# Optimization experiments

Measured on AMD Instinct MI355X. Metric: run time of the kernel, lower is better.

## Reference

```python
import jax, jax.numpy as jnp
import numpy as np
from jax import lax

IN_CH = 32
OUT_CH = 32
K = 7
PAD = 3
STRIDE = 1


def setup_inputs() -> dict:
    key = jax.random.key(0)
    k1, k2, k3 = jax.random.split(key, 3)
    B, T = 4, 4096
    x = jax.random.normal(k1, (B, IN_CH, T), dtype=jnp.float32)
    # weight-generating conv params: [out*in*k, in, k]
    fan_in = IN_CH * K
    W = jax.random.normal(k2, (OUT_CH * IN_CH * K, IN_CH, K), dtype=jnp.float32) / np.sqrt(fan_in).astype(np.float32)
    b = jax.random.normal(k3, (OUT_CH * IN_CH * K,), dtype=jnp.float32) * 0.01
    return {"x": x, "W": W, "b": b}


def _unfold1d(x):
    # x: [B, C, L]; pad then stack K shifted views -> [B, C, K, T]
    xp = jnp.pad(x, ((0, 0), (0, 0), (PAD, PAD)))
    Lp = xp.shape[-1]
    T = Lp - K + 1
    return jnp.stack([xp[:, :, i:i + T:STRIDE] for i in range(K)], axis=2)


def reference(x, W, b):
    B, C, L = x.shape
    # dynamic weight generation: conv1d, same padding -> [B, out*in*K, T]
    dw = lax.conv_general_dilated(
        x, W, window_strides=(STRIDE,), padding=[(PAD, PAD)],
        dimension_numbers=("NCH", "OIH", "NCH"))
    dw = dw + b[None, :, None]
    dw = dw.reshape(B, OUT_CH, IN_CH, K, -1)  # [B, O, I, K, T]
    dw = jax.nn.softmax(dw / np.sqrt(K).astype(np.float32), axis=3)
    x_unf = _unfold1d(x)  # [B, I, K, T]
    y = jnp.einsum("bckt,bockt->bot", x_unf, dw)
    return y
```

## Files before the change

kernel.cpp:

```cpp
#include <hip/hip_runtime.h>
#include <hip/hip_bf16.h>


typedef unsigned short u16;
typedef unsigned int u32;
typedef __attribute__((ext_vector_type(8))) short short8;
typedef __attribute__((ext_vector_type(4))) float f32x4;

#define IN_CH 32
#define OUT_CH 32
#define KW 7
#define TSZ 4096
#define BSZ 4
#define CONTR 224
#define NROWS 7168
#define BLK_T 512
#define XS_STRIDE 40
#define XS_ROWS (BLK_T + 6)
#define SLICE_U16 3584
#define CH_U16 25088
#define CEXP2 0.54528747f

__device__ __forceinline__ u32 f2bf(float v) {
    u32 b = __float_as_uint(v);
    return (b + 0x7fffu + ((b >> 16) & 1u)) >> 16;
}

__device__ __forceinline__ void glds16(const u16* g, u16* l) {
    __builtin_amdgcn_global_load_lds((__attribute__((address_space(1))) void*)g,
                                     (__attribute__((address_space(3))) void*)l,
                                     16, 0, 0);
}

__global__ __launch_bounds__(512)
void wprep(const float* __restrict__ W, const float* __restrict__ bias,
           u16* __restrict__ Wp, float* __restrict__ bp) {
    __shared__ float ws[CH_U16];
    int ch  = blockIdx.x;
    int tid = threadIdx.x;
    const float* src = W + (size_t)ch * CH_U16;
    #pragma unroll
    for (int it = 0; it < 49; ++it)
        ws[it * 512 + tid] = src[it * 512 + tid];
    __syncthreads();
    u16* dst = Wp + (size_t)ch * CH_U16;
    #pragma unroll
    for (int it = 0; it < 49; ++it) {
        int oidx = it * 512 + tid;
        int e  = oidx & 7;
        int pp = (oidx >> 3) & 3;
        int t1 = oidx >> 5;
        int rp = t1 % 112;
        int j  = t1 / 112;
        int p  = pp ^ ((rp >> 1) & 3);
        int c  = p * 8 + e;
        int k  = rp >> 4;
        int q  = rp & 15;
        dst[oidx] = (u16)f2bf(ws[(q * 7 + k) * CONTR + c * 7 + j] * CEXP2);
    }
    if (tid < 112) {
        int k = tid >> 4, q = tid & 15;
        int gp = ch * 16 + q;
        int o = gp >> 5, i = gp & 31;
        bp[ch * 112 + tid] = bias[(o * IN_CH + i) * KW + k] * CEXP2;
    }
}

__global__ __launch_bounds__(256)
void xprep(const float* __restrict__ x, u16* __restrict__ xT) {
    int bid = blockIdx.x;
    int b = bid >> 6;
    int t0 = (bid & 63) * 64;
    __shared__ float lds[32][65];
    int tid = threadIdx.x;
    #pragma unroll
    for (int it = 0; it < 8; ++it) {
        int gi = it * 256 + tid;
        int c = gi >> 6;
        int t = gi & 63;
        lds[c][t] = x[((size_t)b * IN_CH + c) * TSZ + t0 + t];
    }
    __syncthreads();
    #pragma unroll
    for (int it = 0; it < 4; ++it) {
        int wi = it * 256 + tid;
        int t  = wi >> 4;
        int cp = wi & 15;
        u32 b0 = f2bf(lds[cp * 2][t]);
        u32 b1 = f2bf(lds[cp * 2 + 1][t]);
        ((u32*)xT)[((size_t)b * TSZ + t0 + t) * 16 + cp] = b0 | (b1 << 16);
    }
}

__global__ __launch_bounds__(512, 1)
void dconv_main(const u16* __restrict__ Wp, const float* __restrict__ bp,
                const u16* __restrict__ xT, float* __restrict__ out) {
    __shared__ u16 xs[XS_ROWS * XS_STRIDE];
    __shared__ u16 wbuf[2][CH_U16];

    int tid  = threadIdx.x;
    int lane = tid & 63;
    int wave = tid >> 6;
    int g    = lane >> 4;
    int col  = lane & 15;

    int bid = blockIdx.x;
    int b   = bid & 3;
    int tt  = (bid >> 2) & 7;
    int os  = bid >> 5;
    int t0  = tt * BLK_T;

    #pragma unroll
    for (int it = 0; it < 17; ++it) {
        int wi = it * 512 + tid;
        if (wi < XS_ROWS * 16) {
            int row = wi >> 4;
            int cp  = wi & 15;
            int t = t0 - 3 + row;
            u32 v = 0;
            if (t >= 0 && t < TSZ)
                v = ((const u32*)xT)[((size_t)b * TSZ + t) * 16 + cp];
            int sw = ((row >> 3) & 1) << 3;
            *(u32*)&xs[row * XS_STRIDE + ((cp * 2) ^ sw)] = v;
        }
    }

    if (wave < 7) {
        const u16* src = Wp + (size_t)(os * 8) * CH_U16 + wave * SLICE_U16 + lane * 8;
        u16* dst = &wbuf[0][wave * SLICE_U16];
        #pragma unroll
        for (int it = 0; it < 7; ++it) glds16(src + it * 512, dst + it * 512);
    }
    __syncthreads();

    int laneA = col * 32 + ((g ^ ((col >> 1) & 3)) * 8);
    int colw0 = wave * 64 + col;

    float yacc[4] = {0.f, 0.f, 0.f, 0.f};

    #pragma unroll 1
    for (int ci = 0; ci < 8; ++ci) {
        int cur = ci & 1;
        if (ci < 7 && wave < 7) {
            const u16* src = Wp + (size_t)(os * 8 + ci + 1) * CH_U16 + wave * SLICE_U16 + lane * 8;
            u16* dst = &wbuf[cur ^ 1][wave * SLICE_U16];
            #pragma unroll
            for (int it = 0; it < 7; ++it) glds16(src + it * 512, dst + it * 512);
        }

        int ch = os * 8 + ci;
        int cc = ci & 1;

        f32x4 acc[7][4];
        const float* bsrc = bp + ch * 112 + g * 4;
        #pragma unroll
        for (int m = 0; m < 7; ++m) {
            f32x4 bv = *(const f32x4*)(bsrc + m * 16);
            acc[m][0] = bv; acc[m][1] = bv; acc[m][2] = bv; acc[m][3] = bv;
        }

        __builtin_amdgcn_s_setprio(1);
        const u16* wl = &wbuf[cur][laneA];
        #pragma unroll
        for (int j = 0; j < 7; ++j) {
            short8 bf[4];
            #pragma unroll
            for (int ct = 0; ct < 4; ++ct) {
                int row = colw0 + ct * 16 + j;
                int sw = ((row >> 3) & 1) << 3;
                bf[ct] = *(const short8*)&xs[row * XS_STRIDE + ((g * 8) ^ sw)];
            }
            #pragma unroll
            for (int m = 0; m < 7; ++m) {
                short8 af = *(const short8*)(wl + j * SLICE_U16 + m * 512);
                acc[m][0] = __builtin_amdgcn_mfma_f32_16x16x32_bf16(af, bf[0], acc[m][0], 0, 0, 0);
                acc[m][1] = __builtin_amdgcn_mfma_f32_16x16x32_bf16(af, bf[1], acc[m][1], 0, 0, 0);
                acc[m][2] = __builtin_amdgcn_mfma_f32_16x16x32_bf16(af, bf[2], acc[m][2], 0, 0, 0);
                acc[m][3] = __builtin_amdgcn_mfma_f32_16x16x32_bf16(af, bf[3], acc[m][3], 0, 0, 0);
            }
        }
        __builtin_amdgcn_s_setprio(0);

        __syncthreads();

        int ibase = cc * 16 + g * 4;
        #pragma unroll
        for (int ct = 0; ct < 4; ++ct) {
            int colw = colw0 + ct * 16;
            u32 xv0[7], xv1[7];
            #pragma unroll
            for (int k = 0; k < 7; ++k) {
                int row = colw + k;
                int sw = ((row >> 3) & 1) << 3;
                const u32* px = (const u32*)&xs[row * XS_STRIDE + (ibase ^ sw)];
                xv0[k] = px[0]; xv1[k] = px[1];
            }
            #pragma unroll
            for (int r = 0; r < 4; ++r) {
                float ssum = 0.f, psum = 0.f;
                #pragma unroll
                for (int k = 0; k < 7; ++k) {
                    float e = __builtin_amdgcn_exp2f(acc[k][ct][r]);
                    u32 w = (r & 2) ? xv1[k] : xv0[k];
                    float xf = __uint_as_float((r & 1) ? (w & 0xffff0000u) : (w << 16));
                    ssum += e;
                    psum = fmaf(e, xf, psum);
                }
                yacc[ct] += psum * __builtin_amdgcn_rcpf(ssum);
            }
        }

        if (cc == 1) {
            int o = os * 4 + (ci >> 1);
            #pragma unroll
            for (int ct = 0; ct < 4; ++ct) {
                float v = yacc[ct];
                v += __shfl_xor(v, 16, 64);
                v += __shfl_xor(v, 32, 64);
                if (lane < 16)
                    out[((size_t)b * OUT_CH + o) * TSZ + t0 + wave * 64 + ct * 16 + col] = v;
                yacc[ct] = 0.f;
            }
        }
    }
}

extern "C" void kernel_launch(void* const* d_in, const int* in_sizes, int n_in,
                              void* d_out, int out_size, void* d_ws, size_t ws_size,
                              hipStream_t stream) {
    const float* x    = (const float*)d_in[0];
    const float* W    = (const float*)d_in[1];
    const float* bias = (const float*)d_in[2];
    float* out = (float*)d_out;

    u16*   Wp = (u16*)d_ws;
    float* bp = (float*)((char*)d_ws + 3211264);
    u16*   xT = (u16*)((char*)d_ws + 3211264 + 28672);

    hipLaunchKernelGGL(wprep, dim3(64), dim3(512), 0, stream, W, bias, Wp, bp);
    hipLaunchKernelGGL(xprep, dim3(BSZ * (TSZ / 64)), dim3(256), 0, stream, x, xT);
    hipLaunchKernelGGL(dconv_main, dim3(256), dim3(512), 0, stream, Wp, bp, xT, out);
}
```

Before: 122.3 us.

## Interleave weight prefetch with per-tap MFMA phases and permute channel order

Spreads the next-channel weight global→LDS staging across the seven tap iterations instead of issuing it all at the start. Each tap now loads its A/B fragments, waits at a workgroup barrier, then runs its MFMA burst. The channel order is permuted consistently in wprep and xprep so the epilogue can reuse the same LDS addressing as the MFMA B-fragment loads. This aims to overlap weight transfers with compute and keep waves in lockstep, but adds two barriers per tap, which may cost more than it saves.

Result: slower. 132.9 us (+8.6%).

```diff
diff --git a/kernel.cpp b/kernel.cpp
--- a/kernel.cpp
+++ b/kernel.cpp
@@ -53,7 +53,7 @@
         int rp = t1 % 112;
         int j  = t1 / 112;
         int p  = pp ^ ((rp >> 1) & 3);
-        int c  = p * 8 + e;
+        int c  = ((e >> 2) << 4) + (p << 2) + (e & 3);
         int k  = rp >> 4;
         int q  = rp & 15;
         dst[oidx] = (u16)f2bf(ws[(q * 7 + k) * CONTR + c * 7 + j] * CEXP2);
@@ -86,8 +86,10 @@
         int wi = it * 256 + tid;
         int t  = wi >> 4;
         int cp = wi & 15;
-        u32 b0 = f2bf(lds[cp * 2][t]);
-        u32 b1 = f2bf(lds[cp * 2 + 1][t]);
+        int pc = cp * 2;
+        int sc = ((pc & 7) >> 2) * 16 + (pc >> 3) * 4 + (pc & 3);
+        u32 b0 = f2bf(lds[sc][t]);
+        u32 b1 = f2bf(lds[sc + 1][t]);
         ((u32*)xT)[((size_t)b * TSZ + t0 + t) * 16 + cp] = b0 | (b1 << 16);
     }
 }
@@ -141,13 +143,6 @@
     #pragma unroll 1
     for (int ci = 0; ci < 8; ++ci) {
         int cur = ci & 1;
-        if (ci < 7 && wave < 7) {
-            const u16* src = Wp + (size_t)(os * 8 + ci + 1) * CH_U16 + wave * SLICE_U16 + lane * 8;
-            u16* dst = &wbuf[cur ^ 1][wave * SLICE_U16];
-            #pragma unroll
-            for (int it = 0; it < 7; ++it) glds16(src + it * 512, dst + it * 512);
-        }
-
         int ch = os * 8 + ci;
         int cc = ci & 1;
 
@@ -159,11 +154,16 @@
             acc[m][0] = bv; acc[m][1] = bv; acc[m][2] = bv; acc[m][3] = bv;
         }
 
-        __builtin_amdgcn_s_setprio(1);
-        const u16* wl = &wbuf[cur][laneA];
+        const u16* wl   = &wbuf[cur][laneA];
+        const u16* srcN = Wp + (size_t)(os * 8 + ci + 1) * CH_U16 + wave * SLICE_U16 + lane * 8;
+        u16* dstN       = &wbuf[cur ^ 1][wave * SLICE_U16];
+        bool doStage    = (ci < 7) && (wave < 7);
+
         #pragma unroll
         for (int j = 0; j < 7; ++j) {
-            short8 bf[4];
+            if (doStage) glds16(srcN + j * 512, dstN + j * 512);
+
+            short8 bf[4], af[7];
             #pragma unroll
             for (int ct = 0; ct < 4; ++ct) {
                 int row = colw0 + ct * 16 + j;
@@ -171,19 +171,28 @@
                 bf[ct] = *(const short8*)&xs[row * XS_STRIDE + ((g * 8) ^ sw)];
             }
             #pragma unroll
+            for (int m = 0; m < 7; ++m)
+                af[m] = *(const short8*)(wl + j * SLICE_U16 + m * 512);
+
+            __builtin_amdgcn_s_barrier();
+            asm volatile("s_waitcnt lgkmcnt(0)" ::: "memory");
+            __builtin_amdgcn_sched_barrier(0);
+
+            __builtin_amdgcn_s_setprio(1);
+            #pragma unroll
             for (int m = 0; m < 7; ++m) {
-                short8 af = *(const short8*)(wl + j * SLICE_U16 + m * 512);
-                acc[m][0] = __builtin_amdgcn_mfma_f32_16x16x32_bf16(af, bf[0], acc[m][0], 0, 0, 0);
-                acc[m][1] = __builtin_amdgcn_mfma_f32_16x16x32_bf16(af, bf[1], acc[m][1], 0, 0, 0);
-                acc[m][2] = __builtin_amdgcn_mfma_f32_16x16x32_bf16(af, bf[2], acc[m][2], 0, 0, 0);
-                acc[m][3] = __builtin_amdgcn_mfma_f32_16x16x32_bf16(af, bf[3], acc[m][3], 0, 0, 0);
-            }
-        }
-        __builtin_amdgcn_s_setprio(0);
-
-        __syncthreads();
-
-        int ibase = cc * 16 + g * 4;
+                acc[m][0] = __builtin_amdgcn_mfma_f32_16x16x32_bf16(af[m], bf[0], acc[m][0], 0, 0, 0);
+                acc[m][1] = __builtin_amdgcn_mfma_f32_16x16x32_bf16(af[m], bf[1], acc[m][1], 0, 0, 0);
+                acc[m][2] = __builtin_amdgcn_mfma_f32_16x16x32_bf16(af[m], bf[2], acc[m][2], 0, 0, 0);
+                acc[m][3] = __builtin_amdgcn_mfma_f32_16x16x32_bf16(af[m], bf[3], acc[m][3], 0, 0, 0);
+            }
+            __builtin_amdgcn_s_setprio(0);
+            __builtin_amdgcn_s_barrier();
+        }
+
+        asm volatile("s_waitcnt vmcnt(0)" ::: "memory");
+        __builtin_amdgcn_s_barrier();
+
         #pragma unroll
         for (int ct = 0; ct < 4; ++ct) {
             int colw = colw0 + ct * 16;
@@ -192,7 +201,7 @@
             for (int k = 0; k < 7; ++k) {
                 int row = colw + k;
                 int sw = ((row >> 3) & 1) << 3;
-                const u32* px = (const u32*)&xs[row * XS_STRIDE + (ibase ^ sw)];
+                const u32* px = (const u32*)&xs[row * XS_STRIDE + ((g * 8) ^ sw) + cc * 4];
                 xv0[k] = px[0]; xv1[k] = px[1];
             }
             #pragma unroll
```
